# Optimization experiments

Measured on AMD Instinct MI355X. Metric: run time of the kernel, lower is better.

Reference implementation:

```python
import jax, jax.numpy as jnp
import numpy as np

# dims: batch, input channels, hidden neurons, actions, time bins
B, C_IN, HID, OUT, T = 1024, 8, 300, 2, 300
TS, TAU_SR, THETA = 1.0, 10.0, 10.0   # simulation step, SRM kernel tau, spike threshold
TAU_REF, SCALE_REF = 2.0, 2.0          # refractory alpha-kernel tau and scale
TAU_RHO, SCALE_RHO = 1.0, 1.0          # surrogate-gradient pdf params (SLAYER)
K = 100                                 # SRM kernel truncation length (alpha kernel is negligible past 10*tau)

_t = np.arange(K, dtype=np.float32) * TS
SRM = jnp.asarray((_t / TAU_SR) * np.exp(1.0 - _t / TAU_SR))  # alpha PSP kernel, eps(0)=0


def psp(x):
    # slayer.psp: causal temporal convolution of the weighted input with the SRM alpha kernel. x: [B, C, T]
    b, c, t = x.shape
    lhs = x.reshape(b * c, 1, t)
    rhs = SRM[::-1].reshape(1, 1, K).astype(x.dtype)  # flip so correlation == causal convolution
    out = jax.lax.conv_general_dilated(lhs, rhs, (1,), [(K - 1, 0)],
                                       dimension_numbers=('NCH', 'OIH', 'NCH'))
    return out.reshape(b, c, t)


@jax.custom_vjp
def heaviside(u):
    # forward: hard threshold; backward: SLAYER surrogate pdf scaleRho/tauRho * exp(-|u|/tauRho)
    return (u >= 0).astype(u.dtype)

def _hs_fwd(u):
    return heaviside(u), u

def _hs_bwd(u, g):
    return (g * (SCALE_RHO / TAU_RHO) * jnp.exp(-jnp.abs(u) / TAU_RHO),)

heaviside.defvjp(_hs_fwd, _hs_bwd)


def spike(u):
    # slayer.spike: integrate-and-fire with an alpha-shaped refractory response
    # refKernel(n) = -scaleRef*theta * (n*Ts/tauRef) * exp(1 - n*Ts/tauRef)
    # realized exactly via a 2-state linear recurrence (x = n*a^n term, y = a^n term)
    a = jnp.exp(jnp.asarray(-TS / TAU_REF, u.dtype))
    A = jnp.asarray(-SCALE_REF * THETA * np.e * TS / TAU_REF, u.dtype)

    def step(carry, u_t):
        x, y = carry                     # x: accumulated refractory potential at this step
        s = heaviside(u_t + x - THETA)   # membrane (psp + refractory) vs threshold
        y2 = y + A * s                   # spike injects impulse into the alpha-kernel state
        return (a * (x + y2), a * y2), s

    u_tbc = jnp.moveaxis(u, -1, 0)  # [T, B, C]
    z = jnp.zeros(u.shape[:-1], u.dtype)
    _, s = jax.lax.scan(step, (z, z), u_tbc)
    return jnp.moveaxis(s, 0, -1)


def setup_inputs():
    key = jax.random.key(0)
    k1, k2, k3 = jax.random.split(key, 3)
    # CartPoleEncoder output is a spike train: Bernoulli(0.3) spikes over T bins
    encoded_input = (jax.random.uniform(k1, (B, C_IN, T)) < 0.3).astype(jnp.float32)
    W1 = jax.random.normal(k2, (HID, C_IN), dtype=jnp.float32)
    W2 = jax.random.normal(k3, (OUT, HID), dtype=jnp.float32)
    return {"encoded_input": encoded_input, "W1": W1, "W2": W2}


def reference(encoded_input, W1, W2):
    # fc is a 1x1x1 conv3d == per-timestep dense layer over channels
    sl1 = spike(psp(jnp.einsum('bit,oi->bot', encoded_input, W1)))  # [B, 300, T]
    sl2 = spike(psp(jnp.einsum('bht,oh->bot', sl1, W2)))            # [B, 2, T]
    logits = jnp.sum(sl2, axis=-1)                                   # spike counts -> Categorical logits [B, 2]
    g = jax.random.gumbel(jax.random.key(42), logits.shape, logits.dtype)
    pi = jnp.argmax(logits + g, axis=-1)                             # Categorical sample via Gumbel-max
    logp = jax.nn.log_softmax(logits, axis=-1)
    logp_pi = jnp.take_along_axis(logp, pi[:, None], axis=-1)[:, 0]
    return logits, pi, logp_pi
```

## Files before the change

kernel.cpp:

```cpp
#include <hip/hip_runtime.h>
#include <stdint.h>


#define NB    1024
#define CIN   8
#define HID   300
#define TLEN  300
#define KTAP  99
#define THETA 10.0f
#define QMAX  76

#define LDS_K1 142768

__device__ __forceinline__ void threefry2x32(uint32_t c0, uint32_t c1,
                                             uint32_t& o0, uint32_t& o1) {
  const uint32_t k0 = 0u, k1 = 42u;
  const uint32_t k2 = k0 ^ k1 ^ 0x1BD11BDAu;
  uint32_t x0 = c0 + k0, x1 = c1 + k1;
#define TFR(r) { x0 += x1; x1 = (x1 << (r)) | (x1 >> (32 - (r))); x1 ^= x0; }
  TFR(13) TFR(15) TFR(26) TFR(6)  x0 += k1; x1 += k2 + 1u;
  TFR(17) TFR(29) TFR(16) TFR(24) x0 += k2; x1 += k0 + 2u;
  TFR(13) TFR(15) TFR(26) TFR(6)  x0 += k0; x1 += k1 + 3u;
  TFR(17) TFR(29) TFR(16) TFR(24) x0 += k1; x1 += k2 + 4u;
  TFR(13) TFR(15) TFR(26) TFR(6)  x0 += k2; x1 += k0 + 5u;
#undef TFR
  o0 = x0; o1 = x1;
}

__device__ __forceinline__ float jax_uniform_from_bits(uint32_t bits) {
  uint32_t fb = (bits >> 9) | 0x3F800000u;
  float f = __uint_as_float(fb) - 1.0f;
  const float tiny = 1.17549435e-38f;
  float u = __fadd_rn(f, tiny);
  return fmaxf(tiny, u);
}

__global__ void snn_taps_kernel(double* __restrict__ tapsG) {
  const int i = threadIdx.x;
  if (i < 107) {
    const int j = i - 2;
    double v = 0.0;
    if (j >= 1 && j <= KTAP) {
      float q  = (float)j / 10.0f;
      float ef = (float)exp((double)(1.0f - q));
      v = (double)__fmul_rn(q, ef);
    }
    tapsG[i] = v;
  }
}

__global__ __launch_bounds__(1024, 1)
void snn_l1_kernel(const float* __restrict__ enc,
                   const float* __restrict__ W1,
                   const double* __restrict__ tapsG,
                   unsigned long long* __restrict__ maskG) {
  extern __shared__ char smem[];
  float*    xbuf = (float*)(smem);
  float*    ubuf = (float*)(smem + 102656);
  uint32_t* encB = (uint32_t*)(smem + 141568);

  const int tid  = threadIdx.x;
  const int lane = tid & 63;
  const int wv   = tid >> 6;
  const int bh   = blockIdx.x;
  const int b    = blockIdx.y;
  const int h    = bh * 64 + lane;

  if (tid < TLEN) {
    uint32_t m = 0u;
#pragma unroll
    for (int c = 0; c < CIN; ++c)
      if (enc[b * (CIN * TLEN) + c * TLEN + tid] != 0.0f) m |= (1u << c);
    encB[tid] = m;
  }
  for (int i = tid; i < 101 * 64; i += 1024)
    xbuf[i] = 0.0f;
  __syncthreads();

  float w1f[8];
#pragma unroll
  for (int c = 0; c < 8; ++c)
    w1f[c] = (h < HID) ? W1[h * 8 + c] : 0.0f;

  for (int t = wv; t < TLEN; t += 16) {
    const uint32_t bits = encB[t];
    float xf = 0.0f;
#pragma unroll
    for (int c = 0; c < 8; ++c) {
      float wsel = (bits & (1u << c)) ? w1f[c] : 0.0f;
      xf = __fadd_rn(xf, wsel);
    }
    xbuf[(101 + t) * 64 + lane] = xf;
  }
  __syncthreads();

  const float arf = (float)0.6065306597126334;
  const float Af  = (float)-27.182818284590452;

  auto fir_range = [&](int qs, int qlen, int bufsel, int cstart, int cstep) {
    const int nq = qlen >> 2;
#pragma clang loop unroll(disable)
    for (int c = cstart; c < nq; c += cstep) {
      const int t0 = qs + c * 4;
      double a0 = 0.0, a1 = 0.0, a2 = 0.0, a3 = 0.0;
#pragma clang loop unroll(disable)
      for (int g = 0; g < 13; ++g) {
        const int m0 = __builtin_amdgcn_readfirstlane(g << 3);
        const float* xg = xbuf + (96 + t0 - (g << 3)) * 64 + lane;
        float xf[8];
#pragma unroll
        for (int u = 0; u < 8; ++u) xf[u] = xg[u * 64];
        double kt[11];
#pragma unroll
        for (int u = 0; u < 11; ++u) kt[u] = tapsG[m0 + u];
#pragma unroll
        for (int d = 0; d < 8; ++d) {
          const double xv = (double)xf[7 - d];
          a0 += kt[d + 0] * xv;
          a1 += kt[d + 1] * xv;
          a2 += kt[d + 2] * xv;
          a3 += kt[d + 3] * xv;
        }
      }
      float* ub = ubuf + bufsel * (QMAX * 64) + (t0 - qs) * 64 + lane;
      ub[0]   = (float)a0;
      ub[64]  = (float)a1;
      ub[128] = (float)a2;
      ub[192] = (float)a3;
    }
  };

  float RX = 0.0f, RY = 0.0f;
  unsigned long long* maskW = maskG + (size_t)b * (5 * TLEN) + bh * TLEN;

  auto scan_range = [&](int qs, int qlen, int bufsel) {
    const float* ub = ubuf + bufsel * (QMAX * 64) + lane;
#pragma clang loop unroll(disable)
    for (int r = 0; r < qlen; r += 4) {
      float u0 = ub[(r + 0) * 64];
      float u1 = ub[(r + 1) * 64];
      float u2 = ub[(r + 2) * 64];
      float u3 = ub[(r + 3) * 64];
#pragma unroll
      for (int d = 0; d < 4; ++d) {
        float umem = (d == 0) ? u0 : (d == 1) ? u1 : (d == 2) ? u2 : u3;
        float v  = __fsub_rn(__fadd_rn(umem, RX), THETA);
        bool  sp = (v >= 0.0f) && (h < HID);
        unsigned long long bal = __ballot(sp);
        if (lane == 0) maskW[qs + r + d] = bal;
        float sf = sp ? 1.0f : 0.0f;
        float y2 = __fadd_rn(RY, __fmul_rn(Af, sf));
        RX = __fmul_rn(arf, __fadd_rn(RX, y2));
        RY = __fmul_rn(arf, y2);
      }
    }
  };

  const int qs_[5] = {0, 76, 152, 228, 300};
  fir_range(0, 76, 0, wv, 16);
  __syncthreads();
#pragma clang loop unroll(disable)
  for (int q = 0; q < 4; ++q) {
    if (wv == 0) {
      scan_range(qs_[q], qs_[q + 1] - qs_[q], q & 1);
    } else if (q < 3) {
      fir_range(qs_[q + 1], qs_[q + 2] - qs_[q + 1], (q + 1) & 1, wv - 1, 15);
    }
    __syncthreads();
  }
}

__global__ __launch_bounds__(320)
void snn_l2_kernel(const float* __restrict__ W2,
                   const unsigned long long* __restrict__ maskG,
                   float* __restrict__ out) {
  __shared__ double             kD[100];
  __shared__ double             W2D[2 * HID];
  __shared__ unsigned long long maskL[5 * TLEN];
  __shared__ double             zD[2 * 304];
  __shared__ float              u2L[2 * 304];
  __shared__ float              lgL[2];

  const int tid = threadIdx.x;
  const int b   = blockIdx.x;

  const float arf = (float)0.6065306597126334;
  const float Af  = (float)-27.182818284590452;

  for (int j = tid; j < 100; j += 320) {
    float q  = (float)j / 10.0f;
    float ef = (float)exp((double)(1.0f - q));
    kD[j] = (double)__fmul_rn(q, ef);
  }
  for (int i = tid; i < 2 * HID; i += 320)
    W2D[i] = (double)W2[i];
  for (int i = tid; i < 5 * TLEN; i += 320)
    maskL[i] = maskG[(size_t)b * (5 * TLEN) + i];
  __syncthreads();

  if (tid < TLEN) {
    const int t = tid;
    double z0 = 0.0, z1 = 0.0;
#pragma unroll
    for (int w5 = 0; w5 < 5; ++w5) {
      const unsigned long long mm = maskL[w5 * TLEN + t];
      const int kend = (w5 == 4) ? (HID - 256) : 64;
      for (int k = 0; k < kend; ++k) {
        const bool bit = (mm >> k) & 1ull;
        const int  hh  = w5 * 64 + k;
        z0 += bit ? W2D[hh] : 0.0;
        z1 += bit ? W2D[HID + hh] : 0.0;
      }
    }
    zD[t]       = (double)((float)z0);
    zD[304 + t] = (double)((float)z1);
  }
  __syncthreads();

  if (tid < TLEN) {
    const int t = tid;
    double a0 = 0.0, a1 = 0.0;
    const int jmax = (t < KTAP) ? t : KTAP;
    for (int j = 1; j <= jmax; ++j) {
      const double kk = kD[j];
      a0 += kk * zD[t - j];
      a1 += kk * zD[304 + t - j];
    }
    u2L[t]       = (float)a0;
    u2L[304 + t] = (float)a1;
  }
  __syncthreads();

  if (tid < 2) {
    float RX = 0.0f, RY = 0.0f;
    int cnt = 0;
    for (int t = 0; t < TLEN; ++t) {
      float u  = u2L[tid * 304 + t];
      float v  = __fsub_rn(__fadd_rn(u, RX), THETA);
      bool  sp = (v >= 0.0f);
      cnt += sp ? 1 : 0;
      float sf = sp ? 1.0f : 0.0f;
      float y2 = __fadd_rn(RY, __fmul_rn(Af, sf));
      RX = __fmul_rn(arf, __fadd_rn(RX, y2));
      RY = __fmul_rn(arf, y2);
    }
    lgL[tid] = (float)cnt;
  }
  __syncthreads();

  if (tid == 0) {
    float l0 = lgL[0], l1 = lgL[1];
    uint32_t o0, o1;
    threefry2x32(0u, 2u * (uint32_t)b, o0, o1);
    float g0 = -logf(-logf(jax_uniform_from_bits(o0 ^ o1)));
    threefry2x32(0u, 2u * (uint32_t)b + 1u, o0, o1);
    float g1 = -logf(-logf(jax_uniform_from_bits(o0 ^ o1)));

    float v0 = __fadd_rn(l0, g0);
    float v1 = __fadd_rn(l1, g1);
    int   pi = (v1 > v0) ? 1 : 0;
    float m   = fmaxf(l0, l1);
    float s0f = __fsub_rn(l0, m), s1f = __fsub_rn(l1, m);
    float lse = logf(__fadd_rn(expf(s0f), expf(s1f)));
    float lp  = __fsub_rn(pi ? s1f : s0f, lse);

    out[2 * b + 0] = l0;
    out[2 * b + 1] = l1;
    out[2048 + b]  = (float)pi;
    out[3072 + b]  = lp;
  }
}

extern "C" void kernel_launch(void* const* d_in, const int* in_sizes, int n_in,
                              void* d_out, int out_size, void* d_ws, size_t ws_size,
                              hipStream_t stream) {
  const float* enc = (const float*)d_in[0];
  const float* W1  = (const float*)d_in[1];
  const float* W2  = (const float*)d_in[2];
  float* out = (float*)d_out;

  double*             tapsG = (double*)d_ws;
  unsigned long long* maskG = (unsigned long long*)((char*)d_ws + 1024);

  hipFuncSetAttribute((const void*)snn_l1_kernel,
                      hipFuncAttributeMaxDynamicSharedMemorySize, LDS_K1);

  snn_taps_kernel<<<dim3(1), dim3(128), 0, stream>>>(tapsG);
  snn_l1_kernel<<<dim3(5, NB), dim3(1024), LDS_K1, stream>>>(enc, W1, tapsG, maskG);
  snn_l2_kernel<<<dim3(NB), dim3(320), 0, stream>>>(W2, maskG, out);
}
```

Before: 795.9 us.

## Rebalance layer-1 FIR/scan pipeline into five 60-step stages with LDS taps

The layer-1 kernel's FIR/scan pipeline moves from four uneven 76-step stages to five equal 60-step stages. Each of 15 waves now computes exactly one 4-step chunk per stage, so load is balanced and the scan wave handles a shorter first stage. FIR taps are cached in LDS and read as double2 vectors, and the 13-group tap loop is software-pipelined with double-buffered registers. The encoder bitmask packing moves to a separate small kernel writing to the workspace. The trade-offs are an extra kernel launch and pipeline stage, plus higher register pressure from the double buffering.

```diff
diff --git a/kernel.cpp b/kernel.cpp
--- a/kernel.cpp
+++ b/kernel.cpp
@@ -8,9 +8,10 @@
 #define TLEN  300
 #define KTAP  99
 #define THETA 10.0f
-#define QMAX  76
-
-#define LDS_K1 142768
+
+#define LDS_K1 134240
+
+typedef double d2v __attribute__((ext_vector_type(2)));
 
 __device__ __forceinline__ void threefry2x32(uint32_t c0, uint32_t c1,
                                              uint32_t& o0, uint32_t& o1) {
@@ -49,15 +50,27 @@
   }
 }
 
+__global__ __launch_bounds__(320)
+void snn_enc_kernel(const float* __restrict__ enc, uint32_t* __restrict__ encBG) {
+  const int b = blockIdx.x, t = threadIdx.x;
+  if (t < TLEN) {
+    uint32_t m = 0u;
+#pragma unroll
+    for (int c = 0; c < CIN; ++c)
+      if (enc[b * (CIN * TLEN) + c * TLEN + t] != 0.0f) m |= (1u << c);
+    encBG[b * TLEN + t] = m;
+  }
+}
+
 __global__ __launch_bounds__(1024, 1)
-void snn_l1_kernel(const float* __restrict__ enc,
-                   const float* __restrict__ W1,
+void snn_l1_kernel(const float* __restrict__ W1,
                    const double* __restrict__ tapsG,
+                   const uint32_t* __restrict__ encBG,
                    unsigned long long* __restrict__ maskG) {
   extern __shared__ char smem[];
-  float*    xbuf = (float*)(smem);
-  float*    ubuf = (float*)(smem + 102656);
-  uint32_t* encB = (uint32_t*)(smem + 141568);
+  double* kL   = (double*)(smem);
+  float*  xbuf = (float*)(smem + 864);
+  float*  ubuf = (float*)(smem + 103520);
 
   const int tid  = threadIdx.x;
   const int lane = tid & 63;
@@ -66,13 +79,7 @@
   const int b    = blockIdx.y;
   const int h    = bh * 64 + lane;
 
-  if (tid < TLEN) {
-    uint32_t m = 0u;
-#pragma unroll
-    for (int c = 0; c < CIN; ++c)
-      if (enc[b * (CIN * TLEN) + c * TLEN + tid] != 0.0f) m |= (1u << c);
-    encB[tid] = m;
-  }
+  if (tid < 107) kL[tid] = tapsG[tid];
   for (int i = tid; i < 101 * 64; i += 1024)
     xbuf[i] = 0.0f;
   __syncthreads();
@@ -83,7 +90,7 @@
     w1f[c] = (h < HID) ? W1[h * 8 + c] : 0.0f;
 
   for (int t = wv; t < TLEN; t += 16) {
-    const uint32_t bits = encB[t];
+    const uint32_t bits = encBG[__builtin_amdgcn_readfirstlane(b * TLEN + t)];
     float xf = 0.0f;
 #pragma unroll
     for (int c = 0; c < 8; ++c) {
@@ -97,46 +104,58 @@
   const float arf = (float)0.6065306597126334;
   const float Af  = (float)-27.182818284590452;
 
-  auto fir_range = [&](int qs, int qlen, int bufsel, int cstart, int cstep) {
-    const int nq = qlen >> 2;
+#define LOADGRP(g, xf_, kt_) do {                                         \
+    const float* xg_ = xbuf + (96 + t0 - ((g) << 3)) * 64 + lane;         \
+    _Pragma("unroll")                                                     \
+    for (int u_ = 0; u_ < 8; ++u_) xf_[u_] = xg_[u_ * 64];                \
+    const d2v* kp_ = (const d2v*)(kL + ((g) << 3));                       \
+    _Pragma("unroll")                                                     \
+    for (int u_ = 0; u_ < 5; ++u_) {                                      \
+      d2v kv_ = kp_[u_];                                                  \
+      kt_[2 * u_] = kv_.x; kt_[2 * u_ + 1] = kv_.y;                       \
+    }                                                                     \
+    kt_[10] = kL[((g) << 3) + 10];                                        \
+  } while (0)
+
+#define FMAGRP(xf_, kt_) do {                                             \
+    _Pragma("unroll")                                                     \
+    for (int d_ = 0; d_ < 8; ++d_) {                                      \
+      const double xv_ = (double)xf_[7 - d_];                             \
+      a0 += kt_[d_ + 0] * xv_;                                            \
+      a1 += kt_[d_ + 1] * xv_;                                            \
+      a2 += kt_[d_ + 2] * xv_;                                            \
+      a3 += kt_[d_ + 3] * xv_;                                            \
+    }                                                                     \
+  } while (0)
+
+  auto fir_chunk = [&](int s, int c, int bufsel) {
+    const int t0 = 60 * s + 4 * c;
+    double a0 = 0.0, a1 = 0.0, a2 = 0.0, a3 = 0.0;
+    float  xfA[8], xfB[8];
+    double ktA[11], ktB[11];
+    LOADGRP(0, xfA, ktA);
 #pragma clang loop unroll(disable)
-    for (int c = cstart; c < nq; c += cstep) {
-      const int t0 = qs + c * 4;
-      double a0 = 0.0, a1 = 0.0, a2 = 0.0, a3 = 0.0;
-#pragma clang loop unroll(disable)
-      for (int g = 0; g < 13; ++g) {
-        const int m0 = __builtin_amdgcn_readfirstlane(g << 3);
-        const float* xg = xbuf + (96 + t0 - (g << 3)) * 64 + lane;
-        float xf[8];
-#pragma unroll
-        for (int u = 0; u < 8; ++u) xf[u] = xg[u * 64];
-        double kt[11];
-#pragma unroll
-        for (int u = 0; u < 11; ++u) kt[u] = tapsG[m0 + u];
-#pragma unroll
-        for (int d = 0; d < 8; ++d) {
-          const double xv = (double)xf[7 - d];
-          a0 += kt[d + 0] * xv;
-          a1 += kt[d + 1] * xv;
-          a2 += kt[d + 2] * xv;
-          a3 += kt[d + 3] * xv;
-        }
-      }
-      float* ub = ubuf + bufsel * (QMAX * 64) + (t0 - qs) * 64 + lane;
-      ub[0]   = (float)a0;
-      ub[64]  = (float)a1;
-      ub[128] = (float)a2;
-      ub[192] = (float)a3;
-    }
+    for (int g = 0; g < 12; g += 2) {
+      LOADGRP(g + 1, xfB, ktB);
+      FMAGRP(xfA, ktA);
+      LOADGRP(g + 2, xfA, ktA);
+      FMAGRP(xfB, ktB);
+    }
+    FMAGRP(xfA, ktA);
+    float* ub = ubuf + bufsel * (60 * 64) + (4 * c) * 64 + lane;
+    ub[0]   = (float)a0;
+    ub[64]  = (float)a1;
+    ub[128] = (float)a2;
+    ub[192] = (float)a3;
   };
 
   float RX = 0.0f, RY = 0.0f;
   unsigned long long* maskW = maskG + (size_t)b * (5 * TLEN) + bh * TLEN;
 
-  auto scan_range = [&](int qs, int qlen, int bufsel) {
-    const float* ub = ubuf + bufsel * (QMAX * 64) + lane;
+  auto scan_stage = [&](int s) {
+    const float* ub = ubuf + (s & 1) * (60 * 64) + lane;
 #pragma clang loop unroll(disable)
-    for (int r = 0; r < qlen; r += 4) {
+    for (int r = 0; r < 60; r += 4) {
       float u0 = ub[(r + 0) * 64];
       float u1 = ub[(r + 1) * 64];
       float u2 = ub[(r + 2) * 64];
@@ -147,7 +166,7 @@
         float v  = __fsub_rn(__fadd_rn(umem, RX), THETA);
         bool  sp = (v >= 0.0f) && (h < HID);
         unsigned long long bal = __ballot(sp);
-        if (lane == 0) maskW[qs + r + d] = bal;
+        if (lane == 0) maskW[60 * s + r + d] = bal;
         float sf = sp ? 1.0f : 0.0f;
         float y2 = __fadd_rn(RY, __fmul_rn(Af, sf));
         RX = __fmul_rn(arf, __fadd_rn(RX, y2));
@@ -156,18 +175,16 @@
     }
   };
 
-  const int qs_[5] = {0, 76, 152, 228, 300};
-  fir_range(0, 76, 0, wv, 16);
+  if (wv < 15) fir_chunk(0, wv, 0);
   __syncthreads();
 #pragma clang loop unroll(disable)
-  for (int q = 0; q < 4; ++q) {
-    if (wv == 0) {
-      scan_range(qs_[q], qs_[q + 1] - qs_[q], q & 1);
-    } else if (q < 3) {
-      fir_range(qs_[q + 1], qs_[q + 2] - qs_[q + 1], (q + 1) & 1, wv - 1, 15);
-    }
+  for (int s = 0; s < 5; ++s) {
+    if (wv == 0)      scan_stage(s);
+    else if (s < 4)   fir_chunk(s + 1, wv - 1, (s + 1) & 1);
     __syncthreads();
   }
+#undef LOADGRP
+#undef FMAGRP
 }
 
 __global__ __launch_bounds__(320)
@@ -280,12 +297,14 @@
   float* out = (float*)d_out;
 
   double*             tapsG = (double*)d_ws;
-  unsigned long long* maskG = (unsigned long long*)((char*)d_ws + 1024);
+  uint32_t*           encBG = (uint32_t*)((char*)d_ws + 1024);
+  unsigned long long* maskG = (unsigned long long*)((char*)d_ws + 1024 + 1228800);
 
   hipFuncSetAttribute((const void*)snn_l1_kernel,
                       hipFuncAttributeMaxDynamicSharedMemorySize, LDS_K1);
 
   snn_taps_kernel<<<dim3(1), dim3(128), 0, stream>>>(tapsG);
-  snn_l1_kernel<<<dim3(5, NB), dim3(1024), LDS_K1, stream>>>(enc, W1, tapsG, maskG);
+  snn_enc_kernel<<<dim3(NB), dim3(320), 0, stream>>>(enc, encBG);
+  snn_l1_kernel<<<dim3(5, NB), dim3(1024), LDS_K1, stream>>>(W1, tapsG, encBG, maskG);
   snn_l2_kernel<<<dim3(NB), dim3(320), 0, stream>>>(W2, maskG, out);
 }
```

After: 834.5 us. 1.05x slower.
